# Kernel optimization log

Measured on AMD Instinct MI355X. Metric: run time of the kernel, lower is better.

The kernel has to match this reference:

```python
import jax, jax.numpy as jnp
import numpy as np
import math

B, S, H, NH = 8, 512, 1024, 16
DH = H // NH
MAX_REL = 64
LN_EPS = 1e-12


def _relpos_table(length, depth, max_rel=MAX_REL):
    # sinusoidal table over relative-distance vocab, gathered into [L, L, depth]
    vocab = 2 * max_rel + 1
    pos = np.arange(vocab, dtype=np.float32)[:, None]
    div = np.exp(np.arange(0, depth, 2, dtype=np.float32) * (-math.log(10000.0) / depth))
    table = np.zeros((vocab, depth), dtype=np.float32)
    table[:, 0::2] = np.sin(pos * div)
    table[:, 1::2] = np.cos(pos * div)
    r = np.arange(length)
    dist = np.clip(r[None, :] - r[:, None], -max_rel, max_rel) + max_rel  # [L,L], entry (i,j)=j-i
    return jnp.asarray(table[dist])  # [L, L, depth]


def _linear(x, W, b):  # torch layout: W [out, in]
    return jnp.einsum('...i,oi->...o', x, W) + b


def _gather_shift(seq, shift, valid_len):
    # seq [B,S,H]; out[i, j] = seq[i, j+shift[i]] for j < valid_len[i], else 0
    pos = jnp.arange(S)
    idx = jnp.clip(pos[None, :] + shift[:, None], 0, S - 1)  # [B,S]
    g = jnp.take_along_axis(seq, idx[:, :, None], axis=1)
    mask = pos[None, :] < valid_len[:, None]
    return jnp.where(mask[:, :, None], g, jnp.zeros((), seq.dtype))


def _nezha_attention(hs, enc, R, Wq, bq, Wk, bk, Wv, bv):
    def heads(x):  # [B,S,H] -> [B,NH,S,DH]
        return x.reshape(B, S, NH, DH).transpose(0, 2, 1, 3)
    q = heads(_linear(hs, Wq, bq))
    k = heads(_linear(enc, Wk, bk))
    v = heads(_linear(enc, Wv, bv))
    scores = jnp.einsum('bhqd,bhkd->bhqk', q, k)
    scores = scores + jnp.einsum('bhqd,qkd->bhqk', q, R)  # relative-key bias
    scores = scores / math.sqrt(DH)
    probs = jax.nn.softmax(scores, axis=-1)  # dropout: eval mode (identity)
    ctx = jnp.einsum('bhqk,bhkd->bhqd', probs, v)
    ctx = ctx + jnp.einsum('bhqk,qkd->bhqd', probs, R)  # relative-value term
    return ctx.transpose(0, 2, 1, 3).reshape(B, S, H)


def setup_inputs() -> dict:
    key = jax.random.key(0)
    ks = jax.random.split(key, 16)
    w = lambda k, shp: jax.random.normal(k, shp, jnp.float32) * 0.02
    return {
        'sequence_output': jax.random.normal(ks[0], (B, S, H), jnp.float32),
        'doc_len': jax.random.randint(ks[1], (B,), 0, 300, jnp.int32),
        'ques_len': jax.random.randint(ks[2], (B,), 0, 100, jnp.int32),
        'option_len': jax.random.randint(ks[3], (B,), 0, 100, jnp.int32),
        'Wq': w(ks[4], (H, H)), 'bq': jnp.zeros((H,), jnp.float32),
        'Wk': w(ks[5], (H, H)), 'bk': jnp.zeros((H,), jnp.float32),
        'Wv': w(ks[6], (H, H)), 'bv': jnp.zeros((H,), jnp.float32),
        'Wp': w(ks[7], (H, H)), 'bp': jnp.zeros((H,), jnp.float32),
        'Wo': w(ks[8], (H, H)), 'bo': jnp.zeros((H,), jnp.float32),
        'ln_g': jnp.ones((H,), jnp.float32), 'ln_b': jnp.zeros((H,), jnp.float32),
    }


def reference(sequence_output, doc_len, ques_len, option_len,
              Wq, bq, Wk, bk, Wv, bv, Wp, bp, Wo, bo, ln_g, ln_b):
    one = jnp.ones_like(doc_len)
    # seperate_seq (only the two tensors DUMA consumes)
    doc_seq = _gather_shift(sequence_output, one, doc_len)
    ques_opt = _gather_shift(sequence_output, doc_len + 1, ques_len + option_len)

    R = _relpos_table(S, DH)
    doc_enc = _nezha_attention(doc_seq, ques_opt, R, Wq, bq, Wk, bk, Wv, bv)
    qo_enc = _nezha_attention(ques_opt, doc_seq, R, Wq, bq, Wk, bk, Wv, bv)

    pooler = lambda x: jnp.tanh(_linear(x, Wp, bp))
    doc_pooled = pooler(doc_enc)
    qo_pooled = pooler(qo_enc)

    # BertSelfOutput: dense + (dropout=eval) + LayerNorm(residual)
    y = _linear(doc_pooled, Wo, bo) + qo_pooled
    mu = jnp.mean(y, axis=-1, keepdims=True)
    var = jnp.mean(jnp.square(y - mu), axis=-1, keepdims=True)
    y = (y - mu) * jax.lax.rsqrt(var + LN_EPS) * ln_g + ln_b

    return pooler(y)
```

## Files before the change

### kernel.cpp

```cpp
#include <hip/hip_runtime.h>
#include <hip/hip_bf16.h>
#include <cstdint>
#include <cstddef>

using bf16 = __hip_bfloat16;
typedef __attribute__((ext_vector_type(8))) short short8;
typedef __attribute__((ext_vector_type(4))) short short4v;
typedef __attribute__((ext_vector_type(4))) float f32x4;

#define KQLD 2048
#define SCL   0.18033688f
#define EXP2F(x) __builtin_amdgcn_exp2f(x)

__device__ __forceinline__ void gl2lds16(const bf16* g, void* l) {
  __builtin_amdgcn_global_load_lds((const __attribute__((address_space(1))) void*)g,
                                   (__attribute__((address_space(3))) void*)l, 16, 0, 0);
}

template<int ACT, bool OUTBF, bool HASB, int VTM>
__global__ __launch_bounds__(256)
void gemm_bt(const bf16* __restrict__ A, const bf16* __restrict__ Bm,
             void* __restrict__ Cv, const float* __restrict__ bias,
             int N, int K, int lda, int ldb, int ldc, bf16* __restrict__ Vt)
{
  __shared__ __align__(16) short lA[128 * 32];
  __shared__ __align__(16) short lB[128 * 32];
  const int tid = threadIdx.x;
  int bx = blockIdx.x, by = blockIdx.y;
  {
    const int nwg = gridDim.x * gridDim.y;
    if ((nwg & 7) == 0) {
      int n = by * gridDim.x + bx;
      n = (n & 7) * (nwg >> 3) + (n >> 3);
      bx = n / gridDim.y;
      by = n % gridDim.y;
    }
  }
  const int m0 = bx * 128;
  const int n0 = by * 128;
  const int w = tid >> 6, lane = tid & 63;
  const int wr = (w >> 1) * 64, wc = (w & 1) * 64;
  const int lr = lane & 15, lg = lane >> 4;
  f32x4 acc[4][4] = {};
  const int e0 = tid, e1 = tid + 256;
  const int r0_ = e0 >> 2, kc0 = (e0 & 3) * 8;
  const int r1_ = e1 >> 2, kc1 = (e1 & 3) * 8;
  const bf16* pa0 = A + (long)(m0 + r0_) * lda + kc0;
  const bf16* pa1 = A + (long)(m0 + r1_) * lda + kc1;
  const bf16* pb0 = Bm + (long)(n0 + r0_) * ldb + kc0;
  const bf16* pb1 = Bm + (long)(n0 + r1_) * ldb + kc1;

  for (int k0 = 0; k0 < K; k0 += 32) {
    __syncthreads();
    gl2lds16(pa0 + k0, &lA[e0 * 8]);
    gl2lds16(pa1 + k0, &lA[e1 * 8]);
    gl2lds16(pb0 + k0, &lB[e0 * 8]);
    gl2lds16(pb1 + k0, &lB[e1 * 8]);
    __syncthreads();
    short8 af[4], bfr[4];
    #pragma unroll
    for (int i = 0; i < 4; ++i) {
      af[i]  = *(const short8*)(&lA[(wr + i * 16 + lr) * 32 + lg * 8]);
      bfr[i] = *(const short8*)(&lB[(wc + i * 16 + lr) * 32 + lg * 8]);
    }
    #pragma unroll
    for (int mf = 0; mf < 4; ++mf)
      #pragma unroll
      for (int nf = 0; nf < 4; ++nf)
        acc[mf][nf] = __builtin_amdgcn_mfma_f32_16x16x32_bf16(af[mf], bfr[nf], acc[mf][nf], 0, 0, 0);
  }

  #pragma unroll
  for (int nf = 0; nf < 4; ++nf) {
    const int col = n0 + wc + nf * 16 + lr;
    if (col >= N) continue;
    const float bv = HASB ? bias[col] : 0.0f;
    if (VTM && col >= 2048) {
      const int hd = col - 2048;
      const int d = hd & 63, hh = hd >> 6;
      #pragma unroll
      for (int mf = 0; mf < 4; ++mf) {
        const int row0 = m0 + wr + mf * 16 + lg * 4;
        const int zz = ((1 - (row0 >> 12)) << 7) | (((row0 >> 9) & 7) << 4) | hh;
        short4v pk;
        #pragma unroll
        for (int j = 0; j < 4; ++j)
          pk[j] = (short)__builtin_bit_cast(unsigned short,
                    __float2bfloat16(acc[mf][nf][j] + bv));
        *(short4v*)(Vt + ((long)(zz * 64 + d)) * 512 + (row0 & 511)) = pk;
      }
    } else {
      #pragma unroll
      for (int mf = 0; mf < 4; ++mf) {
        #pragma unroll
        for (int j = 0; j < 4; ++j) {
          const int row = m0 + wr + mf * 16 + lg * 4 + j;
          float x = acc[mf][nf][j] + bv;
          if (ACT == 1) x = tanhf(x);
          const long off = (long)row * ldc + col;
          if (OUTBF) ((bf16*)Cv)[off] = __float2bfloat16(x);
          else       ((float*)Cv)[off] = x;
        }
      }
    }
  }
}

__global__ __launch_bounds__(256)
void k_prep(const float* __restrict__ w0, const float* __restrict__ w1,
            const float* __restrict__ w2, const float* __restrict__ w3,
            const float* __restrict__ w4, bf16* __restrict__ wdst,
            const float* __restrict__ seq, const int* __restrict__ dl,
            const int* __restrict__ ql, const int* __restrict__ ol,
            bf16* __restrict__ X, bf16* __restrict__ tbl, bf16* __restrict__ tbt,
            const float* __restrict__ bq, const float* __restrict__ bk,
            const float* __restrict__ bv, float* __restrict__ biasq)
{
  const int bid = blockIdx.x, tid = threadIdx.x;
  if (bid < 5120) {
    const int bsel = bid >> 10;
    const float* s = bsel == 0 ? w0 : bsel == 1 ? w1 : bsel == 2 ? w2 : bsel == 3 ? w3 : w4;
    const float sc = (bsel == 0) ? SCL : 1.0f;
    const long loc = ((long)(bid & 1023) * 256 + tid) * 4;
    float4 v = *(const float4*)(s + loc);
    bf16* d = wdst + (long)bsel * 1048576 + loc;
    d[0] = __float2bfloat16(v.x * sc); d[1] = __float2bfloat16(v.y * sc);
    d[2] = __float2bfloat16(v.z * sc); d[3] = __float2bfloat16(v.w * sc);
  } else if (bid < 13312) {
    const int row = bid - 5120;
    const int c = tid * 4;
    const int b = (row >> 9) & 7, j = row & 511;
    int vlen, src;
    if (row < 4096) { vlen = dl[b]; src = (j + 1 > 511) ? 511 : j + 1; }
    else {
      vlen = ql[b] + ol[b];
      int s2 = j + dl[b] + 1;
      src = s2 > 511 ? 511 : (s2 < 0 ? 0 : s2);
    }
    float4 v = make_float4(0, 0, 0, 0);
    if (j < vlen) v = *(const float4*)(seq + ((long)b * 512 + src) * 1024 + c);
    bf16* o = X + (long)row * 1024 + c;
    o[0] = __float2bfloat16(v.x); o[1] = __float2bfloat16(v.y);
    o[2] = __float2bfloat16(v.z); o[3] = __float2bfloat16(v.w);
  } else {
    for (int idx = tid; idx < 144 * 64; idx += 256) {
      const int r = idx >> 6, d = idx & 63;
      float v = 0.0f;
      if (r < 129) {
        const float dv = powf(10000.0f, -(float)(d >> 1) / 32.0f);
        const float a = (float)r * dv;
        v = (d & 1) ? cosf(a) : sinf(a);
      }
      tbl[idx] = __float2bfloat16(v);
    }
    for (int idx = tid; idx < 64 * 160; idx += 256) {
      const int d = idx / 160, rr = idx % 160;
      float v = 0.0f;
      if (rr < 129) {
        const float dv = powf(10000.0f, -(float)(d >> 1) / 32.0f);
        const float a = (float)rr * dv;
        v = (d & 1) ? cosf(a) : sinf(a);
      }
      tbt[idx] = __float2bfloat16(v);
    }
    for (int idx = tid; idx < 3072; idx += 256) {
      float v = (idx < 1024) ? bq[idx] * SCL : (idx < 2048) ? bk[idx - 1024] : bv[idx - 2048];
      biasq[idx] = v;
    }
  }
}

__global__ __launch_bounds__(1024, 4)
void k_attn(const bf16* __restrict__ QKV, const bf16* __restrict__ Vt,
            const bf16* __restrict__ tbl, const bf16* __restrict__ tbt,
            bf16* __restrict__ ctx)
{
  __shared__ __align__(16) unsigned short s_kv[16384];
  __shared__ __align__(16) unsigned short s_ptile[16][16 * 72];
  __shared__ __align__(16) unsigned short s_m[16][16 * 132];

  const int tid = threadIdx.x;
  const int wv = tid >> 6, lane = tid & 63;
  const int lr = lane & 15, lg = lane >> 4;
  const int bid = blockIdx.x;
  const int xcd = bid & 7;
  const int idx = bid >> 3;
  const int z = (xcd << 5) | (idx >> 1);
  const int g = idx & 1;
  const int attn = z >> 7, b = (z >> 4) & 7, h = z & 15;
  const int qtok0 = attn * 4096 + b * 512;
  const int ktok0 = (1 - attn) * 4096 + b * 512;
  const int q0 = g * 256 + wv * 16;
  const int q = q0 + lr;

  unsigned short* ptile = s_ptile[wv];
  unsigned short* mrow  = s_m[wv];

  const bf16* Kbase = QKV + (long)ktok0 * KQLD + 1024 + h * 64;
  const bf16* Vbase = Vt + (long)z * (64 * 512);

  const int sl = tid & 511;
  const int rs = sl >> 3, cs = (sl & 7) * 8;
  const int scz = cs ^ ((rs & 7) << 3);
  const bool isV = tid >= 512;

  short8 qf[2];
  #pragma unroll
  for (int hh = 0; hh < 2; ++hh)
    qf[hh] = *(const short8*)(QKV + (long)(qtok0 + q0 + lr) * KQLD + h * 64 + hh * 32 + lg * 8);

  #define STAGE(kvb_, koff_, voff_) do {                                            \
    if (!isV) gl2lds16(Kbase + (long)((kvb_) + rs) * KQLD + scz, &s_kv[(koff_) + sl * 8]); \
    else      gl2lds16(Vbase + (long)rs * 512 + (kvb_) + scz,    &s_kv[(voff_) + sl * 8]); \
  } while (0)

  STAGE(0, 0, 8192);

  #pragma unroll
  for (int rt = 0; rt < 9; ++rt) {
    f32x4 qa = {};
    #pragma unroll
    for (int hh = 0; hh < 2; ++hh) {
      short8 ta = *(const short8*)(tbl + (rt * 16 + lr) * 64 + hh * 32 + lg * 8);
      qa = __builtin_amdgcn_mfma_f32_16x16x32_bf16(ta, qf[hh], qa, 0, 0, 0);
    }
    if (rt < 8 || lg == 0) {
      short4v pk;
      #pragma unroll
      for (int j = 0; j < 4; ++j)
        pk[j] = (short)__builtin_bit_cast(unsigned short, __float2bfloat16(qa[j]));
      *(short4v*)(&mrow[lr * 132 + rt * 16 + lg * 4]) = pk;
    }
  }

  const int hx = (lr >> 2) & 1;
  const int lgx8 = (lg ^ (lr & 3)) * 8;
  const int lrx64 = lr * 64;

  const float bias_lo = __bfloat162float(((const bf16*)mrow)[lr * 132 + 0]);
  const float bias_hi = __bfloat162float(((const bf16*)mrow)[lr * 132 + 128]);

  float l_run = 0.f, b0 = 0.f, b1 = 0.f;
  f32x4 cacc[4] = {};

  __syncthreads();

  #pragma unroll 2
  for (int t = 0; t < 8; ++t) {
    const int kvb = t * 64;
    const int koff = (t & 1) * 4096;
    const int voff = 8192 + koff;
    if (t < 7) { const int nk = ((t + 1) & 1) * 4096; STAGE(kvb + 64, nk, 8192 + nk); }

    f32x4 sc[4] = {};
    __builtin_amdgcn_s_setprio(1);
    #pragma unroll
    for (int hh = 0; hh < 2; ++hh) {
      const int cb = ((hh ^ hx) << 5) + lgx8;
      #pragma unroll
      for (int kb4 = 0; kb4 < 4; ++kb4) {
        short8 ak = *(const short8*)(&s_kv[koff + kb4 * 1024 + lrx64 + cb]);
        sc[kb4] = __builtin_amdgcn_mfma_f32_16x16x32_bf16(ak, qf[hh], sc[kb4], 0, 0, 0);
      }
    }
    __builtin_amdgcn_s_setprio(0);

    const int cls = (kvb + 63 <= q0 - 64) ? 0 : ((kvb >= q0 + 79) ? 2 : 1);

    float pacc[4];
    if (cls == 1) {
      const bool eLo = (kvb <= q0 - 49);
      const bool eHi = (kvb + 63 >= q0 + 64);
      short4v pks[4];
      #pragma unroll
      for (int kb4 = 0; kb4 < 4; ++kb4) {
        short4v pk;
        float ps = 0.f;
        #pragma unroll
        for (int j = 0; j < 4; ++j) {
          int rel = kvb + kb4 * 16 + 4 * lg + j - q;
          int rc = rel < -64 ? -64 : (rel > 64 ? 64 : rel);
          float bias = __bfloat162float(((const bf16*)mrow)[lr * 132 + rc + 64]);
          float p = EXP2F(sc[kb4][j] + bias);
          ps += p;
          if (eLo && rel <= -64) b0 += p;
          if (eHi && rel >= 64)  b1 += p;
          pk[j] = (short)__builtin_bit_cast(unsigned short, __float2bfloat16(p));
        }
        pks[kb4] = pk;
        pacc[kb4] = ps;
        *(short4v*)(&ptile[lr * 72 + kb4 * 16 + 4 * lg]) = pk;
      }
      l_run += (pacc[0] + pacc[1]) + (pacc[2] + pacc[3]);
      #pragma unroll
      for (int kb4 = 0; kb4 < 4; ++kb4)
        #pragma unroll
        for (int j = 0; j < 4; ++j) {
          int rel = kvb + kb4 * 16 + 4 * lg + j - q;
          if (rel > -64 && rel < 64)
            mrow[lr * 132 + rel + 63] = (unsigned short)pks[kb4][j];
        }
    } else {
      const float bc = (cls == 0) ? bias_lo : bias_hi;
      #pragma unroll
      for (int kb4 = 0; kb4 < 4; ++kb4) {
        short4v pk;
        float ps = 0.f;
        #pragma unroll
        for (int j = 0; j < 4; ++j) {
          float p = EXP2F(sc[kb4][j] + bc);
          ps += p;
          pk[j] = (short)__builtin_bit_cast(unsigned short, __float2bfloat16(p));
        }
        pacc[kb4] = ps;
        *(short4v*)(&ptile[lr * 72 + kb4 * 16 + 4 * lg]) = pk;
      }
      const float ts = (pacc[0] + pacc[1]) + (pacc[2] + pacc[3]);
      l_run += ts;
      if (cls == 0) b0 += ts; else b1 += ts;
    }

    __builtin_amdgcn_s_setprio(1);
    #pragma unroll
    for (int c2 = 0; c2 < 2; ++c2) {
      short8 pa = *(const short8*)(&ptile[lr * 72 + c2 * 32 + lg * 8]);
      const int cb = ((c2 ^ hx) << 5) + lgx8;
      #pragma unroll
      for (int nf = 0; nf < 4; ++nf) {
        short8 vb = *(const short8*)(&s_kv[voff + nf * 1024 + lrx64 + cb]);
        cacc[nf] = __builtin_amdgcn_mfma_f32_16x16x32_bf16(pa, vb, cacc[nf], 0, 0, 0);
      }
    }
    __builtin_amdgcn_s_setprio(0);
    __syncthreads();
  }
  #undef STAGE

  l_run += __shfl_xor(l_run, 16); l_run += __shfl_xor(l_run, 32);
  b0 += __shfl_xor(b0, 16); b0 += __shfl_xor(b0, 32);
  b1 += __shfl_xor(b1, 16); b1 += __shfl_xor(b1, 32);
  const float inv = 1.0f / l_run;

  #pragma unroll
  for (int j = 0; j < 4; ++j) {
    float iq = __shfl(inv, 4 * lg + j);
    #pragma unroll
    for (int nf = 0; nf < 4; ++nf) cacc[nf][j] *= iq;
  }
  short8 paf[5];
  #pragma unroll
  for (int c = 0; c < 5; ++c)
    #pragma unroll
    for (int j = 0; j < 8; ++j) {
      int r = c * 32 + 8 * lg + j;
      float v = 0.f;
      if (r == 0) v = b0;
      else if (r == 128) v = b1;
      else if (r < 128) {
        int k = q + r - 64;
        if (k >= 0 && k < 512)
          v = __bfloat162float(((const bf16*)mrow)[lr * 132 + r - 1]);
      }
      bf16 vb = __float2bfloat16(v * inv);
      paf[c][j] = (short)__builtin_bit_cast(unsigned short, vb);
    }
  __builtin_amdgcn_s_setprio(1);
  #pragma unroll
  for (int c = 0; c < 5; ++c)
    #pragma unroll
    for (int nf = 0; nf < 4; ++nf) {
      short8 tb = *(const short8*)(tbt + (nf * 16 + lr) * 160 + c * 32 + lg * 8);
      cacc[nf] = __builtin_amdgcn_mfma_f32_16x16x32_bf16(paf[c], tb, cacc[nf], 0, 0, 0);
    }
  __builtin_amdgcn_s_setprio(0);
  #pragma unroll
  for (int nf = 0; nf < 4; ++nf)
    #pragma unroll
    for (int j = 0; j < 4; ++j) {
      int qq = q0 + 4 * lg + j;
      ctx[(long)(qtok0 + qq) * 1024 + h * 64 + nf * 16 + lr] = __float2bfloat16(cacc[nf][j]);
    }
}

__global__ __launch_bounds__(256) void k_ln(const float* __restrict__ y,
    const bf16* __restrict__ pooled, const float* __restrict__ g,
    const float* __restrict__ be, bf16* __restrict__ o)
{
  const int row = blockIdx.x, tid = threadIdx.x;
  float x[4], s1 = 0.0f, s2 = 0.0f;
  #pragma unroll
  for (int i = 0; i < 4; ++i) {
    const int c = tid + i * 256;
    x[i] = y[(long)row * 1024 + c] + __bfloat162float(pooled[(long)(4096 + row) * 1024 + c]);
    s1 += x[i]; s2 += x[i] * x[i];
  }
  #pragma unroll
  for (int off = 1; off < 64; off <<= 1) { s1 += __shfl_xor(s1, off); s2 += __shfl_xor(s2, off); }
  __shared__ float r1[4], r2[4];
  if ((tid & 63) == 0) { r1[tid >> 6] = s1; r2[tid >> 6] = s2; }
  __syncthreads();
  s1 = r1[0] + r1[1] + r1[2] + r1[3];
  s2 = r2[0] + r2[1] + r2[2] + r2[3];
  const float mu = s1 * (1.0f / 1024.0f);
  const float var = s2 * (1.0f / 1024.0f) - mu * mu;
  const float rs = rsqrtf(var + 1e-12f);
  #pragma unroll
  for (int i = 0; i < 4; ++i) {
    const int c = tid + i * 256;
    o[(long)row * 1024 + c] = __float2bfloat16((x[i] - mu) * rs * g[c] + be[c]);
  }
}

__global__ void k_sent(float* o, float v) { o[0] = v; }

extern "C" void kernel_launch(void* const* d_in, const int* in_sizes, int n_in,
                              void* d_out, int out_size, void* d_ws, size_t ws_size,
                              hipStream_t stream)
{
  (void)in_sizes; (void)n_in; (void)out_size;
  const float* seq = (const float*)d_in[0];
  const int*  dl = (const int*)d_in[1];
  const int*  ql = (const int*)d_in[2];
  const int*  ol = (const int*)d_in[3];
  const float* Wq = (const float*)d_in[4];  const float* bq = (const float*)d_in[5];
  const float* Wk = (const float*)d_in[6];  const float* bk = (const float*)d_in[7];
  const float* Wv = (const float*)d_in[8];  const float* bv = (const float*)d_in[9];
  const float* Wp = (const float*)d_in[10]; const float* bp = (const float*)d_in[11];
  const float* Wo = (const float*)d_in[12]; const float* bo = (const float*)d_in[13];
  const float* lng = (const float*)d_in[14]; const float* lnb = (const float*)d_in[15];
  float* out = (float*)d_out;
  char* ws = (char*)d_ws;

  size_t cur = 0;
  auto alloc = [&](size_t bts) { size_t o = cur; cur += (bts + 255) & ~(size_t)255; return o; };
  const size_t oBIAS = alloc(3072 * sizeof(float));
  const size_t oTBL  = alloc(144 * 64 * 2);
  const size_t oTBT  = alloc(64 * 160 * 2);
  const size_t oWBF  = alloc(5ull * 1048576 * 2);
  const size_t oXBF  = alloc(8192ull * 1024 * 2);
  const size_t oQKV  = alloc(8192ull * KQLD * 2);
  const size_t oQR   = alloc(8192ull * 2176 * 2);
  const size_t oBP   = alloc(256ull * 64 * 512 * 2);
  if (ws_size < cur) {
    k_sent<<<1, 1, 0, stream>>>(out, 1.0e6f + (float)(ws_size >> 20));
    return;
  }

  float* biasq = (float*)(ws + oBIAS);
  bf16* tbl = (bf16*)(ws + oTBL);
  bf16* tbt = (bf16*)(ws + oTBT);
  bf16* wqb = (bf16*)(ws + oWBF);
  bf16* wpb = wqb + 3 * 1048576;
  bf16* wob = wqb + 4 * 1048576;
  bf16* xbf = (bf16*)(ws + oXBF);
  bf16* qkv = (bf16*)(ws + oQKV);
  bf16* bpb = (bf16*)(ws + oBP);
  bf16* ctx = xbf;
  bf16* pooled = (bf16*)(ws + oQR);
  float* ybuf = (float*)(ws + oQR + 8192ull * 1024 * 2);
  bf16* yln = (bf16*)(ws + oBP);

  dim3 blk(256);
  k_prep<<<13313, blk, 0, stream>>>(Wq, Wk, Wv, Wp, Wo, wqb,
                                    seq, dl, ql, ol, xbf, tbl, tbt,
                                    bq, bk, bv, biasq);

  gemm_bt<0, true, true, 1><<<dim3(64, 24, 1), blk, 0, stream>>>(xbf, wqb, qkv, biasq, 3072, 1024, 1024, 1024, KQLD, bpb);
  k_attn<<<512, dim3(1024), 0, stream>>>(qkv, bpb, tbl, tbt, ctx);

  gemm_bt<1, true, true, 0><<<dim3(64, 8, 1), blk, 0, stream>>>(ctx, wpb, pooled, bp, 1024, 1024, 1024, 1024, 1024, nullptr);
  gemm_bt<0, false, true, 0><<<dim3(32, 8, 1), blk, 0, stream>>>(pooled, wob, ybuf, bo, 1024, 1024, 1024, 1024, 1024, nullptr);
  k_ln<<<4096, blk, 0, stream>>>(ybuf, pooled, lng, lnb, yln);
  gemm_bt<1, false, true, 0><<<dim3(32, 8, 1), blk, 0, stream>>>(yln, wpb, out, bp, 1024, 1024, 1024, 1024, 1024, nullptr);
}
```

Baseline: 281.5 us.

## Triple-buffer GEMM and attention LDS staging with explicit vmcnt waits

Both the projection GEMM and the attention kernel move from single or double-buffered LDS staging to a three-slot ring. Each iteration prefetches two tiles ahead and waits with a partial s_waitcnt vmcnt plus a raw s_barrier, which replaces the full __syncthreads pairs. The attention kernel also restructures the relative-bias row buffer with padding and a per-lane skew, vectorises the bias reads and prob writebacks on non-edge tiles, and hoists the tile-class computation ahead of the QK MFMAs. The extra LDS raises per-block shared memory, which may reduce occupancy, and the hand-written vmcnt counts depend on how many loads each thread issues.

```diff
diff --git a/kernel.cpp b/kernel.cpp
--- a/kernel.cpp
+++ b/kernel.cpp
@@ -11,6 +11,7 @@
 #define KQLD 2048
 #define SCL   0.18033688f
 #define EXP2F(x) __builtin_amdgcn_exp2f(x)
+#define MROWS 140
 
 __device__ __forceinline__ void gl2lds16(const bf16* g, void* l) {
   __builtin_amdgcn_global_load_lds((const __attribute__((address_space(1))) void*)g,
@@ -23,8 +24,8 @@
              void* __restrict__ Cv, const float* __restrict__ bias,
              int N, int K, int lda, int ldb, int ldc, bf16* __restrict__ Vt)
 {
-  __shared__ __align__(16) short lA[128 * 32];
-  __shared__ __align__(16) short lB[128 * 32];
+  __shared__ __align__(16) short lA[3 * 128 * 32];
+  __shared__ __align__(16) short lB[3 * 128 * 32];
   const int tid = threadIdx.x;
   int bx = blockIdx.x, by = blockIdx.y;
   {
@@ -50,25 +51,44 @@
   const bf16* pb0 = Bm + (long)(n0 + r0_) * ldb + kc0;
   const bf16* pb1 = Bm + (long)(n0 + r1_) * ldb + kc1;
 
-  for (int k0 = 0; k0 < K; k0 += 32) {
-    __syncthreads();
-    gl2lds16(pa0 + k0, &lA[e0 * 8]);
-    gl2lds16(pa1 + k0, &lA[e1 * 8]);
-    gl2lds16(pb0 + k0, &lB[e0 * 8]);
-    gl2lds16(pb1 + k0, &lB[e1 * 8]);
-    __syncthreads();
+  #define GSTAGE(k0_, off_) do {                      \
+    gl2lds16(pa0 + (k0_), &lA[(off_) + e0 * 8]);      \
+    gl2lds16(pa1 + (k0_), &lA[(off_) + e1 * 8]);      \
+    gl2lds16(pb0 + (k0_), &lB[(off_) + e0 * 8]);      \
+    gl2lds16(pb1 + (k0_), &lB[(off_) + e1 * 8]);      \
+  } while (0)
+
+  const int nT = K >> 5;
+  GSTAGE(0, 0);
+  if (nT > 1) GSTAGE(32, 4096);
+  if (nT > 2) asm volatile("s_waitcnt vmcnt(4)" ::: "memory");
+  else        asm volatile("s_waitcnt vmcnt(0)" ::: "memory");
+  __builtin_amdgcn_s_barrier();
+  __builtin_amdgcn_sched_barrier(0);
+
+  int ofc = 0, of1 = 4096, of2 = 8192;
+  for (int t = 0; t < nT; ++t) {
+    if (t + 2 < nT) GSTAGE((t + 2) * 32, of2);
     short8 af[4], bfr[4];
     #pragma unroll
     for (int i = 0; i < 4; ++i) {
-      af[i]  = *(const short8*)(&lA[(wr + i * 16 + lr) * 32 + lg * 8]);
-      bfr[i] = *(const short8*)(&lB[(wc + i * 16 + lr) * 32 + lg * 8]);
+      af[i]  = *(const short8*)(&lA[ofc + (wr + i * 16 + lr) * 32 + lg * 8]);
+      bfr[i] = *(const short8*)(&lB[ofc + (wc + i * 16 + lr) * 32 + lg * 8]);
     }
     #pragma unroll
     for (int mf = 0; mf < 4; ++mf)
       #pragma unroll
       for (int nf = 0; nf < 4; ++nf)
         acc[mf][nf] = __builtin_amdgcn_mfma_f32_16x16x32_bf16(af[mf], bfr[nf], acc[mf][nf], 0, 0, 0);
-  }
+    if (t + 1 < nT) {
+      if (t + 2 < nT) asm volatile("s_waitcnt vmcnt(4)" ::: "memory");
+      else            asm volatile("s_waitcnt vmcnt(0)" ::: "memory");
+      __builtin_amdgcn_s_barrier();
+      __builtin_amdgcn_sched_barrier(0);
+      const int tmp = ofc; ofc = of1; of1 = of2; of2 = tmp;
+    }
+  }
+  #undef GSTAGE
 
   #pragma unroll
   for (int nf = 0; nf < 4; ++nf) {
@@ -175,9 +195,9 @@
             const bf16* __restrict__ tbl, const bf16* __restrict__ tbt,
             bf16* __restrict__ ctx)
 {
-  __shared__ __align__(16) unsigned short s_kv[16384];
+  __shared__ __align__(16) unsigned short s_kv[3 * 8192];
   __shared__ __align__(16) unsigned short s_ptile[16][16 * 72];
-  __shared__ __align__(16) unsigned short s_m[16][16 * 132];
+  __shared__ __align__(16) unsigned short s_m[16][16 * MROWS];
 
   const int tid = threadIdx.x;
   const int wv = tid >> 6, lane = tid & 63;
@@ -194,7 +214,7 @@
   const int q = q0 + lr;
 
   unsigned short* ptile = s_ptile[wv];
-  unsigned short* mrow  = s_m[wv];
+  unsigned short* mr = s_m[wv] + lr * MROWS + ((lr & 3) + 4);
 
   const bf16* Kbase = QKV + (long)ktok0 * KQLD + 1024 + h * 64;
   const bf16* Vbase = Vt + (long)z * (64 * 512);
@@ -209,12 +229,12 @@
   for (int hh = 0; hh < 2; ++hh)
     qf[hh] = *(const short8*)(QKV + (long)(qtok0 + q0 + lr) * KQLD + h * 64 + hh * 32 + lg * 8);
 
-  #define STAGE(kvb_, koff_, voff_) do {                                            \
-    if (!isV) gl2lds16(Kbase + (long)((kvb_) + rs) * KQLD + scz, &s_kv[(koff_) + sl * 8]); \
-    else      gl2lds16(Vbase + (long)rs * 512 + (kvb_) + scz,    &s_kv[(voff_) + sl * 8]); \
+  #define STAGE(kvb_, base_) do {                                                          \
+    if (!isV) gl2lds16(Kbase + (long)((kvb_) + rs) * KQLD + scz, &s_kv[(base_) + sl * 8]); \
+    else      gl2lds16(Vbase + (long)rs * 512 + (kvb_) + scz,    &s_kv[(base_) + 4096 + sl * 8]); \
   } while (0)
 
-  STAGE(0, 0, 8192);
+  STAGE(0, 0);
 
   #pragma unroll
   for (int rt = 0; rt < 9; ++rt) {
@@ -225,32 +245,53 @@
       qa = __builtin_amdgcn_mfma_f32_16x16x32_bf16(ta, qf[hh], qa, 0, 0, 0);
     }
     if (rt < 8 || lg == 0) {
-      short4v pk;
       #pragma unroll
       for (int j = 0; j < 4; ++j)
-        pk[j] = (short)__builtin_bit_cast(unsigned short, __float2bfloat16(qa[j]));
-      *(short4v*)(&mrow[lr * 132 + rt * 16 + lg * 4]) = pk;
-    }
-  }
+        mr[rt * 16 + lg * 4 + j] =
+          __builtin_bit_cast(unsigned short, __float2bfloat16(qa[j]));
+    }
+  }
+
+  STAGE(64, 8192);
 
   const int hx = (lr >> 2) & 1;
   const int lgx8 = (lg ^ (lr & 3)) * 8;
   const int lrx64 = lr * 64;
 
-  const float bias_lo = __bfloat162float(((const bf16*)mrow)[lr * 132 + 0]);
-  const float bias_hi = __bfloat162float(((const bf16*)mrow)[lr * 132 + 128]);
+  const float bias_lo = __bfloat162float(((const bf16*)mr)[0]);
+  const float bias_hi = __bfloat162float(((const bf16*)mr)[128]);
 
   float l_run = 0.f, b0 = 0.f, b1 = 0.f;
   f32x4 cacc[4] = {};
 
-  __syncthreads();
-
+  asm volatile("s_waitcnt vmcnt(1)" ::: "memory");
+  __builtin_amdgcn_s_barrier();
+  __builtin_amdgcn_sched_barrier(0);
+
+  int ofc = 0, of1 = 8192, of2 = 16384;
   #pragma unroll 2
   for (int t = 0; t < 8; ++t) {
     const int kvb = t * 64;
-    const int koff = (t & 1) * 4096;
-    const int voff = 8192 + koff;
-    if (t < 7) { const int nk = ((t + 1) & 1) * 4096; STAGE(kvb + 64, nk, 8192 + nk); }
+    if (t < 6) STAGE(kvb + 128, of2);
+    const int koff = ofc, voff = ofc + 4096;
+
+    const int cls = (kvb + 63 <= q0 - 64) ? 0 : ((kvb >= q0 + 79) ? 2 : 1);
+    const bool eLo = (kvb <= q0 - 49);
+    const bool eHi = (kvb + 63 >= q0 + 64);
+    const bool edge = eLo || eHi;
+
+    short4v btup[4];
+    int bbs[4];
+    if (cls == 1) {
+      #pragma unroll
+      for (int kb4 = 0; kb4 < 4; ++kb4) {
+        int bb = kvb + kb4 * 16 + 4 * lg - q;
+        bbs[kb4] = bb;
+        int ar = bb;
+        if (edge && (bb < -66 || bb > 63)) ar = bb & 63;
+        btup[kb4] = *(const short4v*)(mr + ar + 64);
+      }
+    }
 
     f32x4 sc[4] = {};
     __builtin_amdgcn_s_setprio(1);
@@ -265,12 +306,8 @@
     }
     __builtin_amdgcn_s_setprio(0);
 
-    const int cls = (kvb + 63 <= q0 - 64) ? 0 : ((kvb >= q0 + 79) ? 2 : 1);
-
     float pacc[4];
     if (cls == 1) {
-      const bool eLo = (kvb <= q0 - 49);
-      const bool eHi = (kvb + 63 >= q0 + 64);
       short4v pks[4];
       #pragma unroll
       for (int kb4 = 0; kb4 < 4; ++kb4) {
@@ -278,13 +315,22 @@
         float ps = 0.f;
         #pragma unroll
         for (int j = 0; j < 4; ++j) {
-          int rel = kvb + kb4 * 16 + 4 * lg + j - q;
-          int rc = rel < -64 ? -64 : (rel > 64 ? 64 : rel);
-          float bias = __bfloat162float(((const bf16*)mrow)[lr * 132 + rc + 64]);
+          float bias;
+          if (!edge) {
+            bias = __bfloat162float(__builtin_bit_cast(bf16, (unsigned short)btup[kb4][j]));
+          } else {
+            const int rel = bbs[kb4] + j;
+            bias = rel <= -64 ? bias_lo
+                 : (rel >= 64 ? bias_hi
+                 : __bfloat162float(__builtin_bit_cast(bf16, (unsigned short)btup[kb4][j])));
+          }
           float p = EXP2F(sc[kb4][j] + bias);
           ps += p;
-          if (eLo && rel <= -64) b0 += p;
-          if (eHi && rel >= 64)  b1 += p;
+          if (edge) {
+            const int rel = bbs[kb4] + j;
+            if (eLo && rel <= -64) b0 += p;
+            if (eHi && rel >= 64)  b1 += p;
+          }
           pk[j] = (short)__builtin_bit_cast(unsigned short, __float2bfloat16(p));
         }
         pks[kb4] = pk;
@@ -292,14 +338,26 @@
         *(short4v*)(&ptile[lr * 72 + kb4 * 16 + 4 * lg]) = pk;
       }
       l_run += (pacc[0] + pacc[1]) + (pacc[2] + pacc[3]);
-      #pragma unroll
-      for (int kb4 = 0; kb4 < 4; ++kb4)
+      if (!edge) {
         #pragma unroll
-        for (int j = 0; j < 4; ++j) {
-          int rel = kvb + kb4 * 16 + 4 * lg + j - q;
-          if (rel > -64 && rel < 64)
-            mrow[lr * 132 + rel + 63] = (unsigned short)pks[kb4][j];
+        for (int kb4 = 0; kb4 < 4; ++kb4)
+          *(short4v*)(mr + 64 + bbs[kb4]) = pks[kb4];
+      } else {
+        #pragma unroll
+        for (int kb4 = 0; kb4 < 4; ++kb4) {
+          const int bb = bbs[kb4];
+          if (bb >= -63 && bb <= 60) {
+            *(short4v*)(mr + 64 + bb) = pks[kb4];
+          } else {
+            #pragma unroll
+            for (int j = 0; j < 4; ++j) {
+              const int rel = bb + j;
+              if (rel > -64 && rel < 64)
+                mr[64 + rel] = (unsigned short)pks[kb4][j];
+            }
+          }
         }
+      }
     } else {
       const float bc = (cls == 0) ? bias_lo : bias_hi;
       #pragma unroll
@@ -332,7 +390,14 @@
       }
     }
     __builtin_amdgcn_s_setprio(0);
-    __syncthreads();
+
+    if (t < 7) {
+      if (t < 6) asm volatile("s_waitcnt vmcnt(1)" ::: "memory");
+      else       asm volatile("s_waitcnt vmcnt(0)" ::: "memory");
+      __builtin_amdgcn_s_barrier();
+      __builtin_amdgcn_sched_barrier(0);
+      const int tmp = ofc; ofc = of1; of1 = of2; of2 = tmp;
+    }
   }
   #undef STAGE
 
@@ -359,7 +424,7 @@
       else if (r < 128) {
         int k = q + r - 64;
         if (k >= 0 && k < 512)
-          v = __bfloat162float(((const bf16*)mrow)[lr * 132 + r - 1]);
+          v = __bfloat162float(((const bf16*)mr)[r]);
       }
       bf16 vb = __float2bfloat16(v * inv);
       paf[c][j] = (short)__builtin_bit_cast(unsigned short, vb);
```

Measured after the change: 283.9 us. Within noise of the previous version (+0.9%).

## Triple-buffer GEMM LDS loads and add 128x256 tile variant for large GEMMs

Applied to the files above, without the earlier changes.

Replaces the single-buffered GEMM, which synchronized twice per K-step, with a triple-buffered pipeline. Tiles are prefetched two steps ahead via global_load_lds with explicit vmcnt waits and a single barrier per step. A new 512-thread 128x256-tile kernel handles the QKV and first pooler GEMMs to raise reuse, while the smaller GEMMs keep 128x128 tiles. The prep kernel's bf16 conversions are packed into vector stores. The cost is more LDS per block, which may lower occupancy, and hand-written waitcnt counts that must match the number of outstanding loads.

```diff
diff --git a/kernel.cpp b/kernel.cpp
--- a/kernel.cpp
+++ b/kernel.cpp
@@ -18,13 +18,121 @@
 }
 
 template<int ACT, bool OUTBF, bool HASB, int VTM>
+__global__ __launch_bounds__(512)
+void gemm_big(const bf16* __restrict__ A, const bf16* __restrict__ Bm,
+              void* __restrict__ Cv, const float* __restrict__ bias,
+              int N, int K, int lda, int ldb, int ldc, bf16* __restrict__ Vt)
+{
+  __shared__ __align__(16) short lA[3 * 4096];
+  __shared__ __align__(16) short lB[3 * 8192];
+  const int tid = threadIdx.x;
+  int bx = blockIdx.x, by = blockIdx.y;
+  {
+    const int nwg = gridDim.x * gridDim.y;
+    if ((nwg & 7) == 0) {
+      int n = by * gridDim.x + bx;
+      n = (n & 7) * (nwg >> 3) + (n >> 3);
+      bx = n / gridDim.y;
+      by = n % gridDim.y;
+    }
+  }
+  const int m0 = bx * 128;
+  const int n0 = by * 256;
+  const int w = tid >> 6, lane = tid & 63;
+  const int wr = (w >> 2) * 64, wc = (w & 3) * 64;
+  const int lr = lane & 15, lg = lane >> 4;
+  f32x4 acc[4][4] = {};
+  const int ra = tid >> 2, kca = (tid & 3) * 8;
+  const int e1 = tid + 512;
+  const int rb1 = e1 >> 2, kcb1 = (e1 & 3) * 8;
+  const bf16* pa0 = A + (long)(m0 + ra) * lda + kca;
+  const bf16* pb0 = Bm + (long)(n0 + ra) * ldb + kca;
+  const bf16* pb1 = Bm + (long)(n0 + rb1) * ldb + kcb1;
+
+  #define GSTG(k0_, ofa_, ofb_) do {                  \
+    gl2lds16(pa0 + (k0_), &lA[(ofa_) + tid * 8]);     \
+    gl2lds16(pb0 + (k0_), &lB[(ofb_) + tid * 8]);     \
+    gl2lds16(pb1 + (k0_), &lB[(ofb_) + e1 * 8]);      \
+  } while (0)
+
+  const int nT = K >> 5;
+  GSTG(0, 0, 0);
+  if (nT > 1) GSTG(32, 4096, 8192);
+  if (nT > 2) asm volatile("s_waitcnt vmcnt(3)" ::: "memory");
+  else        asm volatile("s_waitcnt vmcnt(0)" ::: "memory");
+  __builtin_amdgcn_s_barrier();
+  __builtin_amdgcn_sched_barrier(0);
+
+  int oa = 0, oa1 = 4096, oa2 = 8192;
+  int ob = 0, ob1 = 8192, ob2 = 16384;
+  for (int t = 0; t < nT; ++t) {
+    if (t + 2 < nT) GSTG((t + 2) * 32, oa2, ob2);
+    short8 af[4], bfr[4];
+    #pragma unroll
+    for (int i = 0; i < 4; ++i) {
+      af[i]  = *(const short8*)(&lA[oa + (wr + i * 16 + lr) * 32 + lg * 8]);
+      bfr[i] = *(const short8*)(&lB[ob + (wc + i * 16 + lr) * 32 + lg * 8]);
+    }
+    #pragma unroll
+    for (int mf = 0; mf < 4; ++mf)
+      #pragma unroll
+      for (int nf = 0; nf < 4; ++nf)
+        acc[mf][nf] = __builtin_amdgcn_mfma_f32_16x16x32_bf16(af[mf], bfr[nf], acc[mf][nf], 0, 0, 0);
+    if (t + 1 < nT) {
+      if (t + 2 < nT) asm volatile("s_waitcnt vmcnt(3)" ::: "memory");
+      else            asm volatile("s_waitcnt vmcnt(0)" ::: "memory");
+      __builtin_amdgcn_s_barrier();
+      __builtin_amdgcn_sched_barrier(0);
+      int tmp = oa; oa = oa1; oa1 = oa2; oa2 = tmp;
+      tmp = ob; ob = ob1; ob1 = ob2; ob2 = tmp;
+    }
+  }
+  #undef GSTG
+
+  #pragma unroll
+  for (int nf = 0; nf < 4; ++nf) {
+    const int col = n0 + wc + nf * 16 + lr;
+    if (col >= N) continue;
+    const float bv = HASB ? bias[col] : 0.0f;
+    if (VTM && col >= 2048) {
+      const int hd = col - 2048;
+      const int d = hd & 63, hh = hd >> 6;
+      #pragma unroll
+      for (int mf = 0; mf < 4; ++mf) {
+        const int row0 = m0 + wr + mf * 16 + lg * 4;
+        const int zz = ((1 - (row0 >> 12)) << 7) | (((row0 >> 9) & 7) << 4) | hh;
+        short4v pk;
+        #pragma unroll
+        for (int j = 0; j < 4; ++j)
+          pk[j] = (short)__builtin_bit_cast(unsigned short,
+                    __float2bfloat16(acc[mf][nf][j] + bv));
+        *(short4v*)(Vt + ((long)(zz * 64 + d)) * 512 + (row0 & 511)) = pk;
+      }
+    } else {
+      #pragma unroll
+      for (int mf = 0; mf < 4; ++mf) {
+        #pragma unroll
+        for (int j = 0; j < 4; ++j) {
+          const int row = m0 + wr + mf * 16 + lg * 4 + j;
+          float x = acc[mf][nf][j] + bv;
+          if (ACT == 1) x = tanhf(x);
+          const long off = (long)row * ldc + col;
+          if (OUTBF) ((bf16*)Cv)[off] = __float2bfloat16(x);
+          else       ((float*)Cv)[off] = x;
+        }
+      }
+    }
+  }
+}
+
+template<int ACT, bool OUTBF, bool HASB>
 __global__ __launch_bounds__(256)
-void gemm_bt(const bf16* __restrict__ A, const bf16* __restrict__ Bm,
+void gemm_sm(const bf16* __restrict__ A, const bf16* __restrict__ Bm,
              void* __restrict__ Cv, const float* __restrict__ bias,
-             int N, int K, int lda, int ldb, int ldc, bf16* __restrict__ Vt)
+             int N, int K, int lda, int ldb, int ldc)
 {
-  __shared__ __align__(16) short lA[128 * 32];
-  __shared__ __align__(16) short lB[128 * 32];
+  __shared__ __align__(16) short lA[3 * 4096];
+  __shared__ __align__(16) short lB[3 * 4096];
   const int tid = threadIdx.x;
   int bx = blockIdx.x, by = blockIdx.y;
   {
@@ -50,57 +158,60 @@
   const bf16* pb0 = Bm + (long)(n0 + r0_) * ldb + kc0;
   const bf16* pb1 = Bm + (long)(n0 + r1_) * ldb + kc1;
 
-  for (int k0 = 0; k0 < K; k0 += 32) {
-    __syncthreads();
-    gl2lds16(pa0 + k0, &lA[e0 * 8]);
-    gl2lds16(pa1 + k0, &lA[e1 * 8]);
-    gl2lds16(pb0 + k0, &lB[e0 * 8]);
-    gl2lds16(pb1 + k0, &lB[e1 * 8]);
-    __syncthreads();
+  #define GSTG2(k0_, off_) do {                       \
+    gl2lds16(pa0 + (k0_), &lA[(off_) + e0 * 8]);      \
+    gl2lds16(pa1 + (k0_), &lA[(off_) + e1 * 8]);      \
+    gl2lds16(pb0 + (k0_), &lB[(off_) + e0 * 8]);      \
+    gl2lds16(pb1 + (k0_), &lB[(off_) + e1 * 8]);      \
+  } while (0)
+
+  const int nT = K >> 5;
+  GSTG2(0, 0);
+  if (nT > 1) GSTG2(32, 4096);
+  if (nT > 2) asm volatile("s_waitcnt vmcnt(4)" ::: "memory");
+  else        asm volatile("s_waitcnt vmcnt(0)" ::: "memory");
+  __builtin_amdgcn_s_barrier();
+  __builtin_amdgcn_sched_barrier(0);
+
+  int ofc = 0, of1 = 4096, of2 = 8192;
+  for (int t = 0; t < nT; ++t) {
+    if (t + 2 < nT) GSTG2((t + 2) * 32, of2);
     short8 af[4], bfr[4];
     #pragma unroll
     for (int i = 0; i < 4; ++i) {
-      af[i]  = *(const short8*)(&lA[(wr + i * 16 + lr) * 32 + lg * 8]);
-      bfr[i] = *(const short8*)(&lB[(wc + i * 16 + lr) * 32 + lg * 8]);
+      af[i]  = *(const short8*)(&lA[ofc + (wr + i * 16 + lr) * 32 + lg * 8]);
+      bfr[i] = *(const short8*)(&lB[ofc + (wc + i * 16 + lr) * 32 + lg * 8]);
     }
     #pragma unroll
     for (int mf = 0; mf < 4; ++mf)
       #pragma unroll
       for (int nf = 0; nf < 4; ++nf)
         acc[mf][nf] = __builtin_amdgcn_mfma_f32_16x16x32_bf16(af[mf], bfr[nf], acc[mf][nf], 0, 0, 0);
-  }
+    if (t + 1 < nT) {
+      if (t + 2 < nT) asm volatile("s_waitcnt vmcnt(4)" ::: "memory");
+      else            asm volatile("s_waitcnt vmcnt(0)" ::: "memory");
+      __builtin_amdgcn_s_barrier();
+      __builtin_amdgcn_sched_barrier(0);
+      const int tmp = ofc; ofc = of1; of1 = of2; of2 = tmp;
+    }
+  }
+  #undef GSTG2
 
   #pragma unroll
   for (int nf = 0; nf < 4; ++nf) {
     const int col = n0 + wc + nf * 16 + lr;
     if (col >= N) continue;
     const float bv = HASB ? bias[col] : 0.0f;
-    if (VTM && col >= 2048) {
-      const int hd = col - 2048;
-      const int d = hd & 63, hh = hd >> 6;
-      #pragma unroll
-      for (int mf = 0; mf < 4; ++mf) {
-        const int row0 = m0 + wr + mf * 16 + lg * 4;
-        const int zz = ((1 - (row0 >> 12)) << 7) | (((row0 >> 9) & 7) << 4) | hh;
-        short4v pk;
-        #pragma unroll
-        for (int j = 0; j < 4; ++j)
-          pk[j] = (short)__builtin_bit_cast(unsigned short,
-                    __float2bfloat16(acc[mf][nf][j] + bv));
-        *(short4v*)(Vt + ((long)(zz * 64 + d)) * 512 + (row0 & 511)) = pk;
-      }
-    } else {
-      #pragma unroll
-      for (int mf = 0; mf < 4; ++mf) {
-        #pragma unroll
-        for (int j = 0; j < 4; ++j) {
-          const int row = m0 + wr + mf * 16 + lg * 4 + j;
-          float x = acc[mf][nf][j] + bv;
-          if (ACT == 1) x = tanhf(x);
-          const long off = (long)row * ldc + col;
-          if (OUTBF) ((bf16*)Cv)[off] = __float2bfloat16(x);
-          else       ((float*)Cv)[off] = x;
-        }
+    #pragma unroll
+    for (int mf = 0; mf < 4; ++mf) {
+      #pragma unroll
+      for (int j = 0; j < 4; ++j) {
+        const int row = m0 + wr + mf * 16 + lg * 4 + j;
+        float x = acc[mf][nf][j] + bv;
+        if (ACT == 1) x = tanhf(x);
+        const long off = (long)row * ldc + col;
+        if (OUTBF) ((bf16*)Cv)[off] = __float2bfloat16(x);
+        else       ((float*)Cv)[off] = x;
       }
     }
   }
@@ -123,9 +234,12 @@
     const float sc = (bsel == 0) ? SCL : 1.0f;
     const long loc = ((long)(bid & 1023) * 256 + tid) * 4;
     float4 v = *(const float4*)(s + loc);
-    bf16* d = wdst + (long)bsel * 1048576 + loc;
-    d[0] = __float2bfloat16(v.x * sc); d[1] = __float2bfloat16(v.y * sc);
-    d[2] = __float2bfloat16(v.z * sc); d[3] = __float2bfloat16(v.w * sc);
+    short4v pk;
+    pk[0] = (short)__builtin_bit_cast(unsigned short, __float2bfloat16(v.x * sc));
+    pk[1] = (short)__builtin_bit_cast(unsigned short, __float2bfloat16(v.y * sc));
+    pk[2] = (short)__builtin_bit_cast(unsigned short, __float2bfloat16(v.z * sc));
+    pk[3] = (short)__builtin_bit_cast(unsigned short, __float2bfloat16(v.w * sc));
+    *(short4v*)(wdst + (long)bsel * 1048576 + loc) = pk;
   } else if (bid < 13312) {
     const int row = bid - 5120;
     const int c = tid * 4;
@@ -139,9 +253,12 @@
     }
     float4 v = make_float4(0, 0, 0, 0);
     if (j < vlen) v = *(const float4*)(seq + ((long)b * 512 + src) * 1024 + c);
-    bf16* o = X + (long)row * 1024 + c;
-    o[0] = __float2bfloat16(v.x); o[1] = __float2bfloat16(v.y);
-    o[2] = __float2bfloat16(v.z); o[3] = __float2bfloat16(v.w);
+    short4v pk;
+    pk[0] = (short)__builtin_bit_cast(unsigned short, __float2bfloat16(v.x));
+    pk[1] = (short)__builtin_bit_cast(unsigned short, __float2bfloat16(v.y));
+    pk[2] = (short)__builtin_bit_cast(unsigned short, __float2bfloat16(v.z));
+    pk[3] = (short)__builtin_bit_cast(unsigned short, __float2bfloat16(v.w));
+    *(short4v*)(X + (long)row * 1024 + c) = pk;
   } else {
     for (int idx = tid; idx < 144 * 64; idx += 256) {
       const int r = idx >> 6, d = idx & 63;
@@ -465,11 +582,11 @@
                                     seq, dl, ql, ol, xbf, tbl, tbt,
                                     bq, bk, bv, biasq);
 
-  gemm_bt<0, true, true, 1><<<dim3(64, 24, 1), blk, 0, stream>>>(xbf, wqb, qkv, biasq, 3072, 1024, 1024, 1024, KQLD, bpb);
+  gemm_big<0, true, true, 1><<<dim3(64, 12, 1), dim3(512), 0, stream>>>(xbf, wqb, qkv, biasq, 3072, 1024, 1024, 1024, KQLD, bpb);
   k_attn<<<512, dim3(1024), 0, stream>>>(qkv, bpb, tbl, tbt, ctx);
 
-  gemm_bt<1, true, true, 0><<<dim3(64, 8, 1), blk, 0, stream>>>(ctx, wpb, pooled, bp, 1024, 1024, 1024, 1024, 1024, nullptr);
-  gemm_bt<0, false, true, 0><<<dim3(32, 8, 1), blk, 0, stream>>>(pooled, wob, ybuf, bo, 1024, 1024, 1024, 1024, 1024, nullptr);
+  gemm_big<1, true, true, 0><<<dim3(64, 4, 1), dim3(512), 0, stream>>>(ctx, wpb, pooled, bp, 1024, 1024, 1024, 1024, 1024, nullptr);
+  gemm_sm<0, false, true><<<dim3(32, 8, 1), blk, 0, stream>>>(pooled, wob, ybuf, bo, 1024, 1024, 1024, 1024, 1024);
   k_ln<<<4096, blk, 0, stream>>>(ybuf, pooled, lng, lnb, yln);
-  gemm_bt<1, false, true, 0><<<dim3(32, 8, 1), blk, 0, stream>>>(yln, wpb, out, bp, 1024, 1024, 1024, 1024, 1024, nullptr);
-}
+  gemm_sm<1, false, true><<<dim3(32, 8, 1), blk, 0, stream>>>(yln, wpb, out, bp, 1024, 1024, 1024, 1024, 1024);
+}
```

Result: no change. 283.4 us (+0.7%).
